# Kernel tuning notes

Hardware: AMD Instinct MI355X
Metric: run time of the kernel (lower is better)

The kernel has to match this reference:

```python
import jax, jax.numpy as jnp
import numpy as np

B, T, D, F, E, K = 4, 2048, 1024, 2048, 8, 2


def setup_inputs() -> dict:
    key = jax.random.key(0)
    ks = jax.random.split(key, 5)
    s = lambda n: 1.0 / np.sqrt(n)
    return {
        "x": jax.random.normal(ks[0], (B, T, D), jnp.float32),
        "gate_w": jax.random.normal(ks[1], (D, E), jnp.float32) * s(D),
        "gate_b": jnp.zeros((E,), jnp.float32),
        "w1": jax.random.normal(ks[2], (E, D, F), jnp.float32) * s(D),
        "b1": jnp.zeros((E, F), jnp.float32),
        "w2": jax.random.normal(ks[3], (E, F, D), jnp.float32) * s(F),
        "b2": jnp.zeros((E, D), jnp.float32),
    }


def reference(x, gate_w, gate_b, w1, b1, w2, b2):
    # Router: gate logits -> top-k -> softmax over the k selected logits
    logits = x @ gate_w + gate_b                      # [B,T,E]
    top_v, top_i = jax.lax.top_k(logits, K)           # [B,T,K]
    top_w = jax.nn.softmax(top_v, axis=-1)            # [B,T,K]
    # Dense combine weights per expert: w_full[b,t,e] = sum_k top_w * 1[top_i==e]
    one_hot = jax.nn.one_hot(top_i, E, dtype=x.dtype)  # [B,T,K,E]
    w_full = jnp.sum(top_w[..., None] * one_hot, axis=-2)  # [B,T,E]
    # All-experts FFN (batched over expert dim), exact-erf GELU as in nn.GELU()
    h = jax.nn.gelu(jnp.einsum('btd,edf->ebtf', x, w1) + b1[:, None, None, :],
                    approximate=False)                 # [E,B,T,F]
    y = jnp.einsum('ebtf,efd->ebtd', h, w2) + b2[:, None, None, :]  # [E,B,T,D]
    # Weighted combine (zero weight for unselected experts == masked dispatch)
    return jnp.einsum('bte,ebtd->btd', w_full, y)      # [B,T,D]
```

## Files before the change

### kernel.cpp

```cpp
#include <hip/hip_runtime.h>
#include <hip/hip_bf16.h>
#include <math.h>

#define B_ 4
#define T_ 2048
#define D_ 1024
#define F_ 2048
#define E_ 8
#define NT (B_ * T_)
#define NS (NT * 2)
#define CAP (NS + E_ * 128)

typedef __attribute__((ext_vector_type(8))) short short8;
typedef __attribute__((ext_vector_type(4))) float floatx4;

static __device__ __forceinline__ unsigned short f2bf(float f) {
  union { float f; unsigned u; } a; a.f = f;
  unsigned r = a.u + 0x7fffu + ((a.u >> 16) & 1u);
  return (unsigned short)(r >> 16);
}

static __device__ __forceinline__ float bf2f(unsigned u) {
  union { unsigned u; float f; } a; a.u = u << 16; return a.f;
}

static __device__ __forceinline__ void gld16(const unsigned short* g, unsigned short* l) {
  __builtin_amdgcn_global_load_lds(
      (const __attribute__((address_space(1))) void*)g,
      (__attribute__((address_space(3))) void*)l, 16, 0, 0);
}

__global__ void transpose_cvt(const float* __restrict__ in, unsigned short* __restrict__ out,
                              int R, int C) {
  __shared__ float tile[32][33];
  int e = blockIdx.z;
  const float* inp = in + (size_t)e * R * C;
  unsigned short* outp = out + (size_t)e * R * C;
  int c0 = blockIdx.x * 32, r0 = blockIdx.y * 32;
  int tx = threadIdx.x, ty = threadIdx.y;
#pragma unroll
  for (int j = 0; j < 4; j++)
    tile[ty + 8 * j][tx] = inp[(size_t)(r0 + ty + 8 * j) * C + c0 + tx];
  __syncthreads();
#pragma unroll
  for (int j = 0; j < 4; j++)
    outp[(size_t)(c0 + ty + 8 * j) * R + r0 + tx] = f2bf(tile[tx][ty + 8 * j]);
}

__global__ void router_k(const float* __restrict__ x, const float* __restrict__ gw,
                         const float* __restrict__ gb, int* __restrict__ ti,
                         float* __restrict__ tw) {
  int wid = threadIdx.x >> 6, lane = threadIdx.x & 63;
  int t = blockIdx.x * 4 + wid;
  const float* xr = x + (size_t)t * D_;
  float acc[E_];
#pragma unroll
  for (int e = 0; e < E_; e++) acc[e] = 0.f;
#pragma unroll
  for (int it = 0; it < D_ / 64; it++) {
    int d = it * 64 + lane;
    float xv = xr[d];
    const float* g = gw + d * E_;
#pragma unroll
    for (int e = 0; e < E_; e++) acc[e] += xv * g[e];
  }
#pragma unroll
  for (int off = 32; off > 0; off >>= 1)
#pragma unroll
    for (int e = 0; e < E_; e++) acc[e] += __shfl_xor(acc[e], off);
  if (lane == 0) {
    float v[E_];
#pragma unroll
    for (int e = 0; e < E_; e++) v[e] = acc[e] + gb[e];
    int i0 = 0; float v0 = v[0];
#pragma unroll
    for (int e = 1; e < E_; e++) if (v[e] > v0) { v0 = v[e]; i0 = e; }
    int i1 = -1; float v1 = -3.4e38f;
#pragma unroll
    for (int e = 0; e < E_; e++) if (e != i0 && v[e] > v1) { v1 = v[e]; i1 = e; }
    float ex = expf(v1 - v0);
    float w0 = 1.f / (1.f + ex);
    float w1 = ex / (1.f + ex);
    ti[2 * t] = i0; tw[2 * t] = w0;
    ti[2 * t + 1] = i1; tw[2 * t + 1] = w1;
  }
}

__global__ void count_prefix_k(const int* __restrict__ ti, int* __restrict__ offs,
                               int* __restrict__ cursors) {
  __shared__ int scnt[4][E_];
  int tid = threadIdx.x;
  int cnt[E_];
#pragma unroll
  for (int k = 0; k < E_; k++) cnt[k] = 0;
  for (int i = tid; i < NS; i += 256) {
    int e = ti[i];
#pragma unroll
    for (int k = 0; k < E_; k++) cnt[k] += (e == k) ? 1 : 0;
  }
#pragma unroll
  for (int off = 32; off > 0; off >>= 1)
#pragma unroll
    for (int k = 0; k < E_; k++) cnt[k] += __shfl_xor(cnt[k], off);
  int wid = tid >> 6, lane = tid & 63;
  if (lane == 0)
#pragma unroll
    for (int k = 0; k < E_; k++) scnt[wid][k] = cnt[k];
  __syncthreads();
  if (tid == 0) {
    int o = 0;
    for (int k = 0; k < E_; k++) {
      int c = scnt[0][k] + scnt[1][k] + scnt[2][k] + scnt[3][k];
      offs[k] = o;
      cursors[k] = o;
      o += (c + 127) & ~127;
    }
    offs[E_] = o;
  }
}

__global__ void fill_k(int* __restrict__ idx) {
  int s = blockIdx.x * 256 + threadIdx.x;
  if (s < CAP) idx[s] = 0;
}

__global__ void scatter_k(const int* __restrict__ ti, const float* __restrict__ tw,
                          int* __restrict__ cursors, int* __restrict__ idx,
                          int* __restrict__ pos_of) {
  int a = blockIdx.x * 256 + threadIdx.x;
  int lane = threadIdx.x & 63;
  int e = ti[a];
  unsigned long long m[E_];
#pragma unroll
  for (int k = 0; k < E_; k++) m[k] = __ballot(e == k);
  int base = 0;
  if (lane < E_) base = atomicAdd(&cursors[lane], __popcll(m[lane]));
  int myBase = __shfl(base, e);
  unsigned long long m_mine = 0;
#pragma unroll
  for (int k = 0; k < E_; k++) if (e == k) m_mine = m[k];
  int rank = __popcll(m_mine & ((1ull << lane) - 1ull));
  int pos = myBase + rank;
  idx[pos] = a >> 1;
  pos_of[a] = pos;
}

__global__ void gather_k(const float* __restrict__ x, const int* __restrict__ idx,
                         unsigned short* __restrict__ Xg) {
  int s = blockIdx.x;
  int t = idx[s];
  const float4* xr = (const float4*)(x + (size_t)t * D_);
  float4 v = xr[threadIdx.x];
  uint2 p;
  p.x = (unsigned)f2bf(v.x) | ((unsigned)f2bf(v.y) << 16);
  p.y = (unsigned)f2bf(v.z) | ((unsigned)f2bf(v.w) << 16);
  ((uint2*)(Xg + (size_t)s * D_))[threadIdx.x] = p;
}


__global__ __launch_bounds__(256) void gemm1_k(const unsigned short* __restrict__ Xg,
                                               const unsigned short* __restrict__ w1t,
                                               const float* __restrict__ b1,
                                               unsigned short* __restrict__ H,
                                               const int* __restrict__ offs) {
  int slot0 = blockIdx.y * 128;
  if (slot0 >= offs[E_]) return;
  int e = 0;
  while (slot0 >= offs[e + 1]) e++;
  const int K = D_;
  const unsigned short* Bp = w1t + (size_t)e * F_ * D_;
  int n0 = blockIdx.x * 128;

  __shared__ unsigned short lA[128 * 32];
  __shared__ unsigned short lB[128 * 32];

  int tid = threadIdx.x;
  int wid = tid >> 6, lane = tid & 63;
  int wr = wid >> 1, wc = wid & 1;
  int quad = lane >> 4, l15 = lane & 15;
  int sw = (l15 >> 1) & 3;

  int srow = 32 * wid + (lane >> 2);
  int scol = (((lane & 3) ^ ((lane >> 3) & 3))) * 8;
  const unsigned short* gA0 = Xg + (size_t)(slot0 + srow) * K + scol;
  const unsigned short* gA1 = gA0 + (size_t)16 * K;
  const unsigned short* gB0 = Bp + (size_t)(n0 + srow) * K + scol;
  const unsigned short* gB1 = gB0 + (size_t)16 * K;
  unsigned short* lA0 = &lA[(32 * wid) * 32];
  unsigned short* lA1 = &lA[(32 * wid + 16) * 32];
  unsigned short* lB0 = &lB[(32 * wid) * 32];
  unsigned short* lB1 = &lB[(32 * wid + 16) * 32];

  floatx4 acc[4][4];
#pragma unroll
  for (int mi = 0; mi < 4; mi++)
#pragma unroll
    for (int ni = 0; ni < 4; ni++) acc[mi][ni] = (floatx4){0.f, 0.f, 0.f, 0.f};

  for (int k0 = 0; k0 < K; k0 += 32) {
    gld16(gA0 + k0, lA0);
    gld16(gA1 + k0, lA1);
    gld16(gB0 + k0, lB0);
    gld16(gB1 + k0, lB1);
    __syncthreads();
    short8 af[4], bfr[4];
#pragma unroll
    for (int mi = 0; mi < 4; mi++)
      af[mi] = *(const short8*)&lA[(64 * wr + 16 * mi + l15) * 32 + (quad ^ sw) * 8];
#pragma unroll
    for (int ni = 0; ni < 4; ni++)
      bfr[ni] = *(const short8*)&lB[(64 * wc + 16 * ni + l15) * 32 + (quad ^ sw) * 8];
#pragma unroll
    for (int mi = 0; mi < 4; mi++)
#pragma unroll
      for (int ni = 0; ni < 4; ni++)
        acc[mi][ni] = __builtin_amdgcn_mfma_f32_16x16x32_bf16(af[mi], bfr[ni], acc[mi][ni], 0, 0, 0);
    __syncthreads();
  }

  const float* bias = b1 + (size_t)e * F_;
#pragma unroll
  for (int mi = 0; mi < 4; mi++) {
    int row = slot0 + 64 * wr + 16 * mi + quad * 4;
#pragma unroll
    for (int ni = 0; ni < 4; ni++) {
      int col = n0 + 64 * wc + 16 * ni + l15;
      float bv = bias[col];
#pragma unroll
      for (int r = 0; r < 4; r++) {
        float v = acc[mi][ni][r] + bv;
        v = 0.5f * v * (1.f + erff(v * 0.70710678118654752f));
        H[(size_t)(row + r) * F_ + col] = f2bf(v);
      }
    }
  }
}

__global__ __launch_bounds__(256) void gemm2_k(const unsigned short* __restrict__ H,
                                               const unsigned short* __restrict__ w2t,
                                               const float* __restrict__ b2,
                                               unsigned short* __restrict__ Yg,
                                               const int* __restrict__ offs) {
  int slot0 = blockIdx.y * 128;
  if (slot0 >= offs[E_]) return;
  int e = 0;
  while (slot0 >= offs[e + 1]) e++;
  const int K = F_;
  const unsigned short* Bp = w2t + (size_t)e * D_ * F_;
  int n0 = blockIdx.x * 128;

  __shared__ unsigned short lA[128 * 32];
  __shared__ unsigned short lB[128 * 32];

  int tid = threadIdx.x;
  int wid = tid >> 6, lane = tid & 63;
  int wr = wid >> 1, wc = wid & 1;
  int quad = lane >> 4, l15 = lane & 15;
  int sw = (l15 >> 1) & 3;

  int srow = 32 * wid + (lane >> 2);
  int scol = (((lane & 3) ^ ((lane >> 3) & 3))) * 8;
  const unsigned short* gA0 = H + (size_t)(slot0 + srow) * K + scol;
  const unsigned short* gA1 = gA0 + (size_t)16 * K;
  const unsigned short* gB0 = Bp + (size_t)(n0 + srow) * K + scol;
  const unsigned short* gB1 = gB0 + (size_t)16 * K;
  unsigned short* lA0 = &lA[(32 * wid) * 32];
  unsigned short* lA1 = &lA[(32 * wid + 16) * 32];
  unsigned short* lB0 = &lB[(32 * wid) * 32];
  unsigned short* lB1 = &lB[(32 * wid + 16) * 32];

  floatx4 acc[4][4];
#pragma unroll
  for (int mi = 0; mi < 4; mi++)
#pragma unroll
    for (int ni = 0; ni < 4; ni++) acc[mi][ni] = (floatx4){0.f, 0.f, 0.f, 0.f};

  for (int k0 = 0; k0 < K; k0 += 32) {
    gld16(gA0 + k0, lA0);
    gld16(gA1 + k0, lA1);
    gld16(gB0 + k0, lB0);
    gld16(gB1 + k0, lB1);
    __syncthreads();
    short8 af[4], bfr[4];
#pragma unroll
    for (int mi = 0; mi < 4; mi++)
      af[mi] = *(const short8*)&lA[(64 * wr + 16 * mi + l15) * 32 + (quad ^ sw) * 8];
#pragma unroll
    for (int ni = 0; ni < 4; ni++)
      bfr[ni] = *(const short8*)&lB[(64 * wc + 16 * ni + l15) * 32 + (quad ^ sw) * 8];
#pragma unroll
    for (int mi = 0; mi < 4; mi++)
#pragma unroll
      for (int ni = 0; ni < 4; ni++)
        acc[mi][ni] = __builtin_amdgcn_mfma_f32_16x16x32_bf16(af[mi], bfr[ni], acc[mi][ni], 0, 0, 0);
    __syncthreads();
  }

  const float* bias = b2 + (size_t)e * D_;
#pragma unroll
  for (int mi = 0; mi < 4; mi++) {
    int row = slot0 + 64 * wr + 16 * mi + quad * 4;
#pragma unroll
    for (int ni = 0; ni < 4; ni++) {
      int col = n0 + 64 * wc + 16 * ni + l15;
      float bv = bias[col];
#pragma unroll
      for (int r = 0; r < 4; r++) {
        float v = acc[mi][ni][r] + bv;
        Yg[(size_t)(row + r) * D_ + col] = f2bf(v);
      }
    }
  }
}

__global__ void combine_k(const unsigned short* __restrict__ Yg,
                          const int* __restrict__ pos_of,
                          const float* __restrict__ tw, float* __restrict__ out) {
  int t = blockIdx.x;
  int p0 = pos_of[2 * t], p1 = pos_of[2 * t + 1];
  float w0 = tw[2 * t], w1 = tw[2 * t + 1];
  uint2 a = ((const uint2*)(Yg + (size_t)p0 * D_))[threadIdx.x];
  uint2 b = ((const uint2*)(Yg + (size_t)p1 * D_))[threadIdx.x];
  float4 r;
  r.x = w0 * bf2f(a.x & 0xffffu) + w1 * bf2f(b.x & 0xffffu);
  r.y = w0 * bf2f(a.x >> 16)     + w1 * bf2f(b.x >> 16);
  r.z = w0 * bf2f(a.y & 0xffffu) + w1 * bf2f(b.y & 0xffffu);
  r.w = w0 * bf2f(a.y >> 16)     + w1 * bf2f(b.y >> 16);
  ((float4*)(out + (size_t)t * D_))[threadIdx.x] = r;
}

extern "C" void kernel_launch(void* const* d_in, const int* in_sizes, int n_in,
                              void* d_out, int out_size, void* d_ws, size_t ws_size,
                              hipStream_t stream) {
  const float* x  = (const float*)d_in[0];
  const float* gw = (const float*)d_in[1];
  const float* gb = (const float*)d_in[2];
  const float* w1 = (const float*)d_in[3];
  const float* b1 = (const float*)d_in[4];
  const float* w2 = (const float*)d_in[5];
  const float* b2 = (const float*)d_in[6];
  float* out = (float*)d_out;

  char* p = (char*)d_ws;
  unsigned short* w1t = (unsigned short*)p; p += (size_t)E_ * D_ * F_ * 2;
  unsigned short* w2t = (unsigned short*)p; p += (size_t)E_ * D_ * F_ * 2;
  unsigned short* Xg  = (unsigned short*)p; p += (size_t)CAP * D_ * 2;
  unsigned short* H   = (unsigned short*)p; p += (size_t)CAP * F_ * 2;
  int*   idx    = (int*)p; p += (size_t)CAP * 4;
  int*   pos_of = (int*)p; p += (size_t)NS * 4;
  int*   ti     = (int*)p; p += (size_t)NS * 4;
  float* tw     = (float*)p; p += (size_t)NS * 4;
  int* cursors = (int*)p; p += 64;
  int* offs    = (int*)p; p += 64;
  unsigned short* Yg = Xg;

  dim3 tb(32, 8);
  transpose_cvt<<<dim3(F_ / 32, D_ / 32, E_), tb, 0, stream>>>(w1, w1t, D_, F_);
  transpose_cvt<<<dim3(D_ / 32, F_ / 32, E_), tb, 0, stream>>>(w2, w2t, F_, D_);
  router_k<<<NT / 4, 256, 0, stream>>>(x, gw, gb, ti, tw);
  count_prefix_k<<<1, 256, 0, stream>>>(ti, offs, cursors);
  fill_k<<<(CAP + 255) / 256, 256, 0, stream>>>(idx);
  scatter_k<<<NS / 256, 256, 0, stream>>>(ti, tw, cursors, idx, pos_of);
  gather_k<<<CAP, 256, 0, stream>>>(x, idx, Xg);
  gemm1_k<<<dim3(F_ / 128, CAP / 128), 256, 0, stream>>>(Xg, w1t, b1, H, offs);
  gemm2_k<<<dim3(D_ / 128, CAP / 128), 256, 0, stream>>>(H, w2t, b2, Yg, offs);
  combine_k<<<NT, 256, 0, stream>>>(Yg, pos_of, tw, out);
}
```

Baseline: 479.1 us.

## Double K-tile depth in grouped GEMMs, new LDS swizzle, and fast GELU approximation

Merges the two expert GEMM kernels into one template and raises the K step per iteration from 32 to 64, with an 8-way XOR swizzle for the larger LDS tiles. This halves the number of barrier pairs per tile and issues more loads per sync. The exact erff GELU is replaced by the Abramowitz-Stegun polynomial built on hardware rcp and exp2, cutting epilogue cost. That polynomial has about 1e-7 absolute error, well within bf16 output precision. The larger LDS footprint (32 KB per block) may reduce occupancy.

```diff
diff --git a/kernel.cpp b/kernel.cpp
--- a/kernel.cpp
+++ b/kernel.cpp
@@ -28,6 +28,20 @@
   __builtin_amdgcn_global_load_lds(
       (const __attribute__((address_space(1))) void*)g,
       (__attribute__((address_space(3))) void*)l, 16, 0, 0);
+}
+
+static __device__ __forceinline__ float gelu_f(float v) {
+  float ax = fabsf(v) * 0.70710678118654752f;
+  float t = __builtin_amdgcn_rcpf(1.f + 0.3275911f * ax);
+  float e = __builtin_amdgcn_exp2f(-ax * ax * 1.44269504088896f);
+  float p = t * (0.254829592f +
+            t * (-0.284496736f +
+            t * (1.421413741f +
+            t * (-1.453152027f +
+            t * 1.061405429f))));
+  float er = 1.f - p * e;
+  er = copysignf(er, v);
+  return 0.5f * v * (1.f + er);
 }
 
 __global__ void transpose_cvt(const float* __restrict__ in, unsigned short* __restrict__ out,
@@ -157,39 +171,32 @@
   ((uint2*)(Xg + (size_t)s * D_))[threadIdx.x] = p;
 }
 
-
-__global__ __launch_bounds__(256) void gemm1_k(const unsigned short* __restrict__ Xg,
-                                               const unsigned short* __restrict__ w1t,
-                                               const float* __restrict__ b1,
-                                               unsigned short* __restrict__ H,
-                                               const int* __restrict__ offs) {
+template <int K, int N, bool GELU>
+__global__ __launch_bounds__(256) void gemm_k(const unsigned short* __restrict__ A,
+                                              const unsigned short* __restrict__ W,
+                                              const float* __restrict__ bias_all,
+                                              unsigned short* __restrict__ O,
+                                              const int* __restrict__ offs) {
   int slot0 = blockIdx.y * 128;
   if (slot0 >= offs[E_]) return;
   int e = 0;
   while (slot0 >= offs[e + 1]) e++;
-  const int K = D_;
-  const unsigned short* Bp = w1t + (size_t)e * F_ * D_;
+  const unsigned short* Bp = W + (size_t)e * N * K;
   int n0 = blockIdx.x * 128;
 
-  __shared__ unsigned short lA[128 * 32];
-  __shared__ unsigned short lB[128 * 32];
+  __shared__ unsigned short lA[128 * 64];
+  __shared__ unsigned short lB[128 * 64];
 
   int tid = threadIdx.x;
   int wid = tid >> 6, lane = tid & 63;
   int wr = wid >> 1, wc = wid & 1;
   int quad = lane >> 4, l15 = lane & 15;
-  int sw = (l15 >> 1) & 3;
-
-  int srow = 32 * wid + (lane >> 2);
-  int scol = (((lane & 3) ^ ((lane >> 3) & 3))) * 8;
-  const unsigned short* gA0 = Xg + (size_t)(slot0 + srow) * K + scol;
-  const unsigned short* gA1 = gA0 + (size_t)16 * K;
-  const unsigned short* gB0 = Bp + (size_t)(n0 + srow) * K + scol;
-  const unsigned short* gB1 = gB0 + (size_t)16 * K;
-  unsigned short* lA0 = &lA[(32 * wid) * 32];
-  unsigned short* lA1 = &lA[(32 * wid + 16) * 32];
-  unsigned short* lB0 = &lB[(32 * wid) * 32];
-  unsigned short* lB1 = &lB[(32 * wid + 16) * 32];
+  int l7 = l15 & 7;
+
+  int sr = lane >> 3;
+  int ch = (lane & 7) ^ sr;
+  const unsigned short* gA = A + (size_t)(slot0 + 32 * wid + sr) * K + ch * 8;
+  const unsigned short* gB = Bp + (size_t)(n0 + 32 * wid + sr) * K + ch * 8;
 
   floatx4 acc[4][4];
 #pragma unroll
@@ -197,28 +204,36 @@
 #pragma unroll
     for (int ni = 0; ni < 4; ni++) acc[mi][ni] = (floatx4){0.f, 0.f, 0.f, 0.f};
 
-  for (int k0 = 0; k0 < K; k0 += 32) {
-    gld16(gA0 + k0, lA0);
-    gld16(gA1 + k0, lA1);
-    gld16(gB0 + k0, lB0);
-    gld16(gB1 + k0, lB1);
+  for (int k0 = 0; k0 < K; k0 += 64) {
+#pragma unroll
+    for (int j = 0; j < 4; j++) {
+      gld16(gA + k0 + (size_t)8 * j * K, &lA[(32 * wid + 8 * j) * 64]);
+      gld16(gB + k0 + (size_t)8 * j * K, &lB[(32 * wid + 8 * j) * 64]);
+    }
     __syncthreads();
-    short8 af[4], bfr[4];
-#pragma unroll
-    for (int mi = 0; mi < 4; mi++)
-      af[mi] = *(const short8*)&lA[(64 * wr + 16 * mi + l15) * 32 + (quad ^ sw) * 8];
-#pragma unroll
-    for (int ni = 0; ni < 4; ni++)
-      bfr[ni] = *(const short8*)&lB[(64 * wc + 16 * ni + l15) * 32 + (quad ^ sw) * 8];
-#pragma unroll
-    for (int mi = 0; mi < 4; mi++)
-#pragma unroll
-      for (int ni = 0; ni < 4; ni++)
-        acc[mi][ni] = __builtin_amdgcn_mfma_f32_16x16x32_bf16(af[mi], bfr[ni], acc[mi][ni], 0, 0, 0);
+#pragma unroll
+    for (int sub = 0; sub < 2; sub++) {
+      short8 af[4], bfr[4];
+#pragma unroll
+      for (int mi = 0; mi < 4; mi++) {
+        int row = 64 * wr + 16 * mi + l15;
+        af[mi] = *(const short8*)&lA[row * 64 + ((((sub << 2) | quad)) ^ l7) * 8];
+      }
+#pragma unroll
+      for (int ni = 0; ni < 4; ni++) {
+        int row = 64 * wc + 16 * ni + l15;
+        bfr[ni] = *(const short8*)&lB[row * 64 + ((((sub << 2) | quad)) ^ l7) * 8];
+      }
+#pragma unroll
+      for (int mi = 0; mi < 4; mi++)
+#pragma unroll
+        for (int ni = 0; ni < 4; ni++)
+          acc[mi][ni] = __builtin_amdgcn_mfma_f32_16x16x32_bf16(af[mi], bfr[ni], acc[mi][ni], 0, 0, 0);
+    }
     __syncthreads();
   }
 
-  const float* bias = b1 + (size_t)e * F_;
+  const float* bias = bias_all + (size_t)e * N;
 #pragma unroll
   for (int mi = 0; mi < 4; mi++) {
     int row = slot0 + 64 * wr + 16 * mi + quad * 4;
@@ -229,85 +244,8 @@
 #pragma unroll
       for (int r = 0; r < 4; r++) {
         float v = acc[mi][ni][r] + bv;
-        v = 0.5f * v * (1.f + erff(v * 0.70710678118654752f));
-        H[(size_t)(row + r) * F_ + col] = f2bf(v);
-      }
-    }
-  }
-}
-
-__global__ __launch_bounds__(256) void gemm2_k(const unsigned short* __restrict__ H,
-                                               const unsigned short* __restrict__ w2t,
-                                               const float* __restrict__ b2,
-                                               unsigned short* __restrict__ Yg,
-                                               const int* __restrict__ offs) {
-  int slot0 = blockIdx.y * 128;
-  if (slot0 >= offs[E_]) return;
-  int e = 0;
-  while (slot0 >= offs[e + 1]) e++;
-  const int K = F_;
-  const unsigned short* Bp = w2t + (size_t)e * D_ * F_;
-  int n0 = blockIdx.x * 128;
-
-  __shared__ unsigned short lA[128 * 32];
-  __shared__ unsigned short lB[128 * 32];
-
-  int tid = threadIdx.x;
-  int wid = tid >> 6, lane = tid & 63;
-  int wr = wid >> 1, wc = wid & 1;
-  int quad = lane >> 4, l15 = lane & 15;
-  int sw = (l15 >> 1) & 3;
-
-  int srow = 32 * wid + (lane >> 2);
-  int scol = (((lane & 3) ^ ((lane >> 3) & 3))) * 8;
-  const unsigned short* gA0 = H + (size_t)(slot0 + srow) * K + scol;
-  const unsigned short* gA1 = gA0 + (size_t)16 * K;
-  const unsigned short* gB0 = Bp + (size_t)(n0 + srow) * K + scol;
-  const unsigned short* gB1 = gB0 + (size_t)16 * K;
-  unsigned short* lA0 = &lA[(32 * wid) * 32];
-  unsigned short* lA1 = &lA[(32 * wid + 16) * 32];
-  unsigned short* lB0 = &lB[(32 * wid) * 32];
-  unsigned short* lB1 = &lB[(32 * wid + 16) * 32];
-
-  floatx4 acc[4][4];
-#pragma unroll
-  for (int mi = 0; mi < 4; mi++)
-#pragma unroll
-    for (int ni = 0; ni < 4; ni++) acc[mi][ni] = (floatx4){0.f, 0.f, 0.f, 0.f};
-
-  for (int k0 = 0; k0 < K; k0 += 32) {
-    gld16(gA0 + k0, lA0);
-    gld16(gA1 + k0, lA1);
-    gld16(gB0 + k0, lB0);
-    gld16(gB1 + k0, lB1);
-    __syncthreads();
-    short8 af[4], bfr[4];
-#pragma unroll
-    for (int mi = 0; mi < 4; mi++)
-      af[mi] = *(const short8*)&lA[(64 * wr + 16 * mi + l15) * 32 + (quad ^ sw) * 8];
-#pragma unroll
-    for (int ni = 0; ni < 4; ni++)
-      bfr[ni] = *(const short8*)&lB[(64 * wc + 16 * ni + l15) * 32 + (quad ^ sw) * 8];
-#pragma unroll
-    for (int mi = 0; mi < 4; mi++)
-#pragma unroll
-      for (int ni = 0; ni < 4; ni++)
-        acc[mi][ni] = __builtin_amdgcn_mfma_f32_16x16x32_bf16(af[mi], bfr[ni], acc[mi][ni], 0, 0, 0);
-    __syncthreads();
-  }
-
-  const float* bias = b2 + (size_t)e * D_;
-#pragma unroll
-  for (int mi = 0; mi < 4; mi++) {
-    int row = slot0 + 64 * wr + 16 * mi + quad * 4;
-#pragma unroll
-    for (int ni = 0; ni < 4; ni++) {
-      int col = n0 + 64 * wc + 16 * ni + l15;
-      float bv = bias[col];
-#pragma unroll
-      for (int r = 0; r < 4; r++) {
-        float v = acc[mi][ni][r] + bv;
-        Yg[(size_t)(row + r) * D_ + col] = f2bf(v);
+        if (GELU) v = gelu_f(v);
+        O[(size_t)(row + r) * N + col] = f2bf(v);
       }
     }
   }
@@ -362,7 +300,7 @@
   fill_k<<<(CAP + 255) / 256, 256, 0, stream>>>(idx);
   scatter_k<<<NS / 256, 256, 0, stream>>>(ti, tw, cursors, idx, pos_of);
   gather_k<<<CAP, 256, 0, stream>>>(x, idx, Xg);
-  gemm1_k<<<dim3(F_ / 128, CAP / 128), 256, 0, stream>>>(Xg, w1t, b1, H, offs);
-  gemm2_k<<<dim3(D_ / 128, CAP / 128), 256, 0, stream>>>(H, w2t, b2, Yg, offs);
+  gemm_k<D_, F_, true><<<dim3(F_ / 128, CAP / 128), 256, 0, stream>>>(Xg, w1t, b1, H, offs);
+  gemm_k<F_, D_, false><<<dim3(D_ / 128, CAP / 128), 256, 0, stream>>>(H, w2t, b2, Yg, offs);
   combine_k<<<NT, 256, 0, stream>>>(Yg, pos_of, tw, out);
 }
```

New measurement: 476.1 us. About the same (-0.6%).
